# Kernel tuning notes

Measured on AMD Instinct MI355X. Metric: run time of the kernel, lower is better.

Reference implementation:

```python
import jax, jax.numpy as jnp
import numpy as np

ENC_DIM, DEC_DIM, ATT_DIM = 512, 512, 256
B, T = 64, 4096


def setup_inputs() -> dict:
    key = jax.random.key(0)
    ks = jax.random.split(key, 7)
    s_enc = 1.0 / np.sqrt(ENC_DIM)
    s_dec = 1.0 / np.sqrt(DEC_DIM)
    s_att = 1.0 / np.sqrt(ATT_DIM)
    return {
        "encoder_features": jax.random.normal(ks[0], (B, T, ENC_DIM), jnp.float32),
        "decoder_hidden": jax.random.normal(ks[1], (B, DEC_DIM), jnp.float32),
        # encoder_proj: Linear(encoder_dim, attention_dim) with bias
        "W_enc": jax.random.uniform(ks[2], (ENC_DIM, ATT_DIM), jnp.float32, -s_enc, s_enc),
        "b_enc": jax.random.uniform(ks[3], (ATT_DIM,), jnp.float32, -s_enc, s_enc),
        # decoder_proj: Linear(decoder_dim, attention_dim, bias=False)
        "W_dec": jax.random.uniform(ks[4], (DEC_DIM, ATT_DIM), jnp.float32, -s_dec, s_dec),
        # attention_vector: Linear(attention_dim, 1) with bias
        "v_att": jax.random.uniform(ks[5], (ATT_DIM,), jnp.float32, -s_att, s_att),
        "b_att": jax.random.uniform(ks[6], (), jnp.float32, -s_att, s_att),
    }


def reference(encoder_features, decoder_hidden, W_enc, b_enc, W_dec, v_att, b_att):
    # (B,T,A) = (B,T,E)@(E,A) + b
    enc_proj = jnp.einsum("bte,ea->bta", encoder_features, W_enc) + b_enc
    # (B,1,A)
    dec_proj = (decoder_hidden @ W_dec)[:, None, :]
    energy = jnp.tanh(enc_proj + dec_proj)                      # (B,T,A)
    scores = jnp.einsum("bta,a->bt", energy, v_att) + b_att     # (B,T)
    attention_weights = jax.nn.softmax(scores, axis=1)          # (B,T)
    context = jnp.einsum("bt,bte->be", attention_weights, encoder_features)
    return (context, attention_weights)
```

## Files before the change

kernel.cpp:

```cpp
#include <hip/hip_runtime.h>
#include <hip/hip_bf16.h>

#define E_DIM 512
#define D_DIM 512
#define A_DIM 256
#define B_SZ  64
#define T_SZ  4096
#define TT    64
#define NTB   (T_SZ / TT)
#define LDT   (E_DIM + 8)

typedef __bf16 bf16_t;
typedef bf16_t bf16x8 __attribute__((ext_vector_type(8)));
typedef float  f32x4  __attribute__((ext_vector_type(4)));

__device__ __forceinline__ unsigned short f2bf(float x) {
    union { float f; unsigned int u; } v; v.f = x;
    unsigned int u = v.u;
    return (unsigned short)((u + 0x7FFFu + ((u >> 16) & 1u)) >> 16);
}
__device__ __forceinline__ float bf_lo(unsigned int pk) {
    union { unsigned int u; float f; } v; v.u = pk << 16; return v.f;
}
__device__ __forceinline__ float bf_hi(unsigned int pk) {
    union { unsigned int u; float f; } v; v.u = pk & 0xFFFF0000u; return v.f;
}
__device__ __forceinline__ float tanh_fast(float x) {
    x = fminf(8.0f, fmaxf(-8.0f, x));
    float e = __expf(2.0f * x);
    return 1.0f - 2.0f * __builtin_amdgcn_rcpf(e + 1.0f);
}

__global__ __launch_bounds__(256) void prep_kernel(
    const float* __restrict__ dec, const float* __restrict__ W_enc,
    const float* __restrict__ b_enc, const float* __restrict__ W_dec,
    float* __restrict__ dp, unsigned short* __restrict__ Wt)
{
    const int bid = blockIdx.x, tid = threadIdx.x;
    if (bid < B_SZ) {
        float s = b_enc[tid];
        const float* dr = dec + bid * D_DIM;
        #pragma unroll 8
        for (int d = 0; d < D_DIM; ++d)
            s = fmaf(dr[d], W_dec[d * A_DIM + tid], s);
        dp[bid * A_DIM + tid] = s;
    } else {
        int base = (bid - B_SZ) * 2048;
        #pragma unroll
        for (int i = 0; i < 8; ++i) {
            int idx = base + tid + i * 256;
            int a = idx >> 9, e = idx & 511;
            Wt[idx] = f2bf(W_enc[e * A_DIM + a]);
        }
    }
}

__global__ __launch_bounds__(512, 4) void attn_main(
    const float* __restrict__ enc, const unsigned short* __restrict__ Wt,
    const float* __restrict__ dpg, const float* __restrict__ vatt,
    float* __restrict__ u_out, float* __restrict__ ctx_part)
{
    const int tb = blockIdx.x, b = blockIdx.y;
    const int tid = threadIdx.x;
    __shared__ unsigned short tile[TT * LDT];
    __shared__ float spart[8][TT];
    __shared__ float uu[TT];
    __shared__ float dp_s[A_DIM];
    __shared__ float vv[A_DIM];
    __shared__ float ctx_red[E_DIM];

    if (tid < A_DIM) {
        dp_s[tid] = dpg[b * A_DIM + tid];
        vv[tid]   = vatt[tid];
    }

    const float4* src = (const float4*)(enc + ((size_t)b * T_SZ + (size_t)tb * TT) * E_DIM);
    #pragma unroll 4
    for (int it = 0; it < 16; ++it) {
        int idx = tid + it * 512;
        int r = idx >> 7, c = idx & 127;
        float4 v4 = src[idx];
        ushort4 h;
        h.x = f2bf(v4.x); h.y = f2bf(v4.y); h.z = f2bf(v4.z); h.w = f2bf(v4.w);
        *(ushort4*)&tile[r * LDT + c * 4] = h;
    }
    __syncthreads();

    const int w = tid >> 6, lane = tid & 63;
    const int m16 = lane & 15, q = lane >> 4;
    f32x4 acc[4][2];
    #pragma unroll
    for (int mi = 0; mi < 4; ++mi)
        #pragma unroll
        for (int ni = 0; ni < 2; ++ni)
            acc[mi][ni] = (f32x4){0.f, 0.f, 0.f, 0.f};

    const unsigned short* WtW = Wt + (size_t)(w * 32) * E_DIM;
    #pragma unroll 2
    for (int k0 = 0; k0 < E_DIM; k0 += 32) {
        const int ka = k0 + q * 8;
        bf16x8 afr[4], bfr[2];
        #pragma unroll
        for (int ni = 0; ni < 2; ++ni)
            bfr[ni] = *(const bf16x8*)&WtW[(ni * 16 + m16) * E_DIM + ka];
        #pragma unroll
        for (int mi = 0; mi < 4; ++mi)
            afr[mi] = *(const bf16x8*)&tile[(mi * 16 + m16) * LDT + ka];
        #pragma unroll
        for (int mi = 0; mi < 4; ++mi)
            #pragma unroll
            for (int ni = 0; ni < 2; ++ni)
                acc[mi][ni] = __builtin_amdgcn_mfma_f32_16x16x32_bf16(
                    afr[mi], bfr[ni], acc[mi][ni], 0, 0, 0);
    }

    float va[2], dpv[2];
    #pragma unroll
    for (int ni = 0; ni < 2; ++ni) {
        int a = w * 32 + ni * 16 + m16;
        va[ni] = vv[a]; dpv[ni] = dp_s[a];
    }
    #pragma unroll
    for (int mi = 0; mi < 4; ++mi) {
        #pragma unroll
        for (int r = 0; r < 4; ++r) {
            float p = va[0] * tanh_fast(acc[mi][0][r] + dpv[0])
                    + va[1] * tanh_fast(acc[mi][1][r] + dpv[1]);
            p += __shfl_xor(p, 1); p += __shfl_xor(p, 2);
            p += __shfl_xor(p, 4); p += __shfl_xor(p, 8);
            if (m16 == 0) spart[w][mi * 16 + q * 4 + r] = p;
        }
    }
    __syncthreads();

    if (tid < TT) {
        float s = 0.f;
        #pragma unroll
        for (int w8 = 0; w8 < 8; ++w8) s += spart[w8][tid];
        float e = __expf(s);
        uu[tid] = e;
        u_out[(size_t)b * T_SZ + (size_t)tb * TT + tid] = e;
    }
    __syncthreads();

    {
        const int c2 = tid & 255, h = tid >> 8;
        float c0 = 0.f, c1 = 0.f;
        #pragma unroll 8
        for (int i = 0; i < 32; ++i) {
            int t = h * 32 + i;
            float ut = uu[t];
            unsigned int pk = *(const unsigned int*)&tile[t * LDT + 2 * c2];
            c0 = fmaf(ut, bf_lo(pk), c0);
            c1 = fmaf(ut, bf_hi(pk), c1);
        }
        if (h == 1) { ctx_red[2 * c2] = c0; ctx_red[2 * c2 + 1] = c1; }
        __syncthreads();
        if (h == 0) {
            c0 += ctx_red[2 * c2];
            c1 += ctx_red[2 * c2 + 1];
            float2 st; st.x = c0; st.y = c1;
            ((float2*)(ctx_part + ((size_t)tb * B_SZ + b) * E_DIM))[c2] = st;
        }
    }
}

__global__ __launch_bounds__(256) void finalize_kernel(
    const float* __restrict__ u, const float* __restrict__ ctx_part,
    float* __restrict__ out)
{
    const int b = blockIdx.x, tid = threadIdx.x;
    __shared__ float red[256];
    const float* ub = u + (size_t)b * T_SZ;
    float s = 0.f;
    for (int i = tid; i < T_SZ; i += 256) s += ub[i];
    red[tid] = s; __syncthreads();
    for (int st = 128; st > 0; st >>= 1) {
        if (tid < st) red[tid] += red[tid + st];
        __syncthreads();
    }
    const float invS = 1.0f / red[0];
    float* wout = out + B_SZ * E_DIM + (size_t)b * T_SZ;
    for (int i = tid; i < T_SZ; i += 256) wout[i] = ub[i] * invS;
    for (int e = tid; e < E_DIM; e += 256) {
        float c = 0.f;
        #pragma unroll 8
        for (int t = 0; t < NTB; ++t)
            c += ctx_part[((size_t)t * B_SZ + b) * E_DIM + e];
        out[(size_t)b * E_DIM + e] = c * invS;
    }
}

extern "C" void kernel_launch(void* const* d_in, const int* in_sizes, int n_in,
                              void* d_out, int out_size, void* d_ws, size_t ws_size,
                              hipStream_t stream) {
    const float* enc   = (const float*)d_in[0];
    const float* dec   = (const float*)d_in[1];
    const float* W_enc = (const float*)d_in[2];
    const float* b_enc = (const float*)d_in[3];
    const float* W_dec = (const float*)d_in[4];
    const float* v_att = (const float*)d_in[5];
    float* out = (float*)d_out;

    char* ws = (char*)d_ws;
    unsigned short* Wt = (unsigned short*)(ws);
    float* dp          = (float*)(ws + 262144);
    float* u           = (float*)(ws + 327680);
    float* ctx_part    = (float*)(ws + 1376256);

    prep_kernel<<<128, 256, 0, stream>>>(dec, W_enc, b_enc, W_dec, dp, Wt);
    attn_main<<<dim3(NTB, B_SZ), 512, 0, stream>>>(enc, Wt, dp, v_att, u, ctx_part);
    finalize_kernel<<<B_SZ, 256, 0, stream>>>(u, ctx_part, out);
}
```

Baseline: 836.3 us.

## Make attention blocks persistent over T slices with double-buffered tiles and atomic reduction

Each block now handles 16 consecutive 32-row tiles of one batch row instead of a single 64-row tile. The next tile's global load is issued into registers while the current tile is processed, then written into a double-buffered LDS tile. Context partials and the softmax denominator go to global memory through atomics, with zeroing done in prep, so the finalize kernel only scales. The grid drops to 512 blocks, which costs parallelism and latency hiding, and the float atomics make the summation order nondeterministic.

```diff
diff --git a/kernel.cpp b/kernel.cpp
--- a/kernel.cpp
+++ b/kernel.cpp
@@ -6,8 +6,10 @@
 #define A_DIM 256
 #define B_SZ  64
 #define T_SZ  4096
-#define TT    64
+#define TT    32
 #define NTB   (T_SZ / TT)
+#define TPB   16
+#define SLICES (NTB / TPB)
 #define LDT   (E_DIM + 8)
 
 typedef __bf16 bf16_t;
@@ -19,11 +21,8 @@
     unsigned int u = v.u;
     return (unsigned short)((u + 0x7FFFu + ((u >> 16) & 1u)) >> 16);
 }
-__device__ __forceinline__ float bf_lo(unsigned int pk) {
-    union { unsigned int u; float f; } v; v.u = pk << 16; return v.f;
-}
-__device__ __forceinline__ float bf_hi(unsigned int pk) {
-    union { unsigned int u; float f; } v; v.u = pk & 0xFFFF0000u; return v.f;
+__device__ __forceinline__ float bf2f(unsigned short h) {
+    union { unsigned int u; float f; } v; v.u = ((unsigned int)h) << 16; return v.f;
 }
 __device__ __forceinline__ float tanh_fast(float x) {
     x = fminf(8.0f, fmaxf(-8.0f, x));
@@ -34,7 +33,8 @@
 __global__ __launch_bounds__(256) void prep_kernel(
     const float* __restrict__ dec, const float* __restrict__ W_enc,
     const float* __restrict__ b_enc, const float* __restrict__ W_dec,
-    float* __restrict__ dp, unsigned short* __restrict__ Wt)
+    float* __restrict__ dp, unsigned short* __restrict__ Wt,
+    float* __restrict__ ctx_acc, float* __restrict__ S)
 {
     const int bid = blockIdx.x, tid = threadIdx.x;
     if (bid < B_SZ) {
@@ -44,6 +44,9 @@
         for (int d = 0; d < D_DIM; ++d)
             s = fmaf(dr[d], W_dec[d * A_DIM + tid], s);
         dp[bid * A_DIM + tid] = s;
+        ctx_acc[bid * E_DIM + tid]       = 0.0f;
+        ctx_acc[bid * E_DIM + 256 + tid] = 0.0f;
+        if (tid == 0) S[bid] = 0.0f;
     } else {
         int base = (bid - B_SZ) * 2048;
         #pragma unroll
@@ -58,136 +61,150 @@
 __global__ __launch_bounds__(512, 4) void attn_main(
     const float* __restrict__ enc, const unsigned short* __restrict__ Wt,
     const float* __restrict__ dpg, const float* __restrict__ vatt,
-    float* __restrict__ u_out, float* __restrict__ ctx_part)
+    float* __restrict__ u_out, float* __restrict__ ctx_acc,
+    float* __restrict__ S)
 {
-    const int tb = blockIdx.x, b = blockIdx.y;
+    const int p = blockIdx.x;
+    const int b = p >> 3, slice = p & 7;
     const int tid = threadIdx.x;
-    __shared__ unsigned short tile[TT * LDT];
+
+    __shared__ unsigned short tile[2][TT * LDT];
     __shared__ float spart[8][TT];
     __shared__ float uu[TT];
     __shared__ float dp_s[A_DIM];
     __shared__ float vv[A_DIM];
-    __shared__ float ctx_red[E_DIM];
 
     if (tid < A_DIM) {
         dp_s[tid] = dpg[b * A_DIM + tid];
         vv[tid]   = vatt[tid];
     }
 
-    const float4* src = (const float4*)(enc + ((size_t)b * T_SZ + (size_t)tb * TT) * E_DIM);
-    #pragma unroll 4
-    for (int it = 0; it < 16; ++it) {
-        int idx = tid + it * 512;
-        int r = idx >> 7, c = idx & 127;
-        float4 v4 = src[idx];
-        ushort4 h;
-        h.x = f2bf(v4.x); h.y = f2bf(v4.y); h.z = f2bf(v4.z); h.w = f2bf(v4.w);
-        *(ushort4*)&tile[r * LDT + c * 4] = h;
-    }
-    __syncthreads();
-
     const int w = tid >> 6, lane = tid & 63;
     const int m16 = lane & 15, q = lane >> 4;
-    f32x4 acc[4][2];
+
+    const float4* src0 = (const float4*)(enc +
+        ((size_t)b * T_SZ + (size_t)slice * TPB * TT) * E_DIM);
+
+    float4 r[8];
     #pragma unroll
-    for (int mi = 0; mi < 4; ++mi)
+    for (int it = 0; it < 8; ++it) r[it] = src0[tid + it * 512];
+    #pragma unroll
+    for (int it = 0; it < 8; ++it) {
+        int idx = tid + it * 512;
+        int rr = idx >> 7, cc = idx & 127;
+        ushort4 h;
+        h.x = f2bf(r[it].x); h.y = f2bf(r[it].y);
+        h.z = f2bf(r[it].z); h.w = f2bf(r[it].w);
+        *(ushort4*)&tile[0][rr * LDT + cc * 4] = h;
+    }
+    __syncthreads();
+
+    float va0, va1, dv0, dv1;
+    {
+        int a0 = w * 32 + m16;
+        va0 = vv[a0]; va1 = vv[a0 + 16];
+        dv0 = dp_s[a0]; dv1 = dp_s[a0 + 16];
+    }
+
+    const unsigned short* WtW = Wt + (size_t)(w * 32) * E_DIM;
+
+    float c_acc = 0.0f;
+    float sS    = 0.0f;
+
+    for (int i = 0; i < TPB; ++i) {
+        const int cur = i & 1, nxt = cur ^ 1;
+
+        if (i + 1 < TPB) {
+            const float4* srcn = src0 + (size_t)(i + 1) * 4096;
+            #pragma unroll
+            for (int it = 0; it < 8; ++it) r[it] = srcn[tid + it * 512];
+        }
+
+        f32x4 acc[2][2];
         #pragma unroll
-        for (int ni = 0; ni < 2; ++ni)
-            acc[mi][ni] = (f32x4){0.f, 0.f, 0.f, 0.f};
-
-    const unsigned short* WtW = Wt + (size_t)(w * 32) * E_DIM;
-    #pragma unroll 2
-    for (int k0 = 0; k0 < E_DIM; k0 += 32) {
-        const int ka = k0 + q * 8;
-        bf16x8 afr[4], bfr[2];
+        for (int mi = 0; mi < 2; ++mi)
+            #pragma unroll
+            for (int ni = 0; ni < 2; ++ni)
+                acc[mi][ni] = (f32x4){0.f, 0.f, 0.f, 0.f};
+
+        #pragma unroll 4
+        for (int k0 = 0; k0 < E_DIM; k0 += 32) {
+            const int ka = k0 + q * 8;
+            bf16x8 afr0 = *(const bf16x8*)&tile[cur][(m16) * LDT + ka];
+            bf16x8 afr1 = *(const bf16x8*)&tile[cur][(16 + m16) * LDT + ka];
+            bf16x8 bfr0 = *(const bf16x8*)&WtW[(m16) * E_DIM + ka];
+            bf16x8 bfr1 = *(const bf16x8*)&WtW[(16 + m16) * E_DIM + ka];
+            acc[0][0] = __builtin_amdgcn_mfma_f32_16x16x32_bf16(afr0, bfr0, acc[0][0], 0, 0, 0);
+            acc[0][1] = __builtin_amdgcn_mfma_f32_16x16x32_bf16(afr0, bfr1, acc[0][1], 0, 0, 0);
+            acc[1][0] = __builtin_amdgcn_mfma_f32_16x16x32_bf16(afr1, bfr0, acc[1][0], 0, 0, 0);
+            acc[1][1] = __builtin_amdgcn_mfma_f32_16x16x32_bf16(afr1, bfr1, acc[1][1], 0, 0, 0);
+        }
+
         #pragma unroll
-        for (int ni = 0; ni < 2; ++ni)
-            bfr[ni] = *(const bf16x8*)&WtW[(ni * 16 + m16) * E_DIM + ka];
-        #pragma unroll
-        for (int mi = 0; mi < 4; ++mi)
-            afr[mi] = *(const bf16x8*)&tile[(mi * 16 + m16) * LDT + ka];
-        #pragma unroll
-        for (int mi = 0; mi < 4; ++mi)
-            #pragma unroll
-            for (int ni = 0; ni < 2; ++ni)
-                acc[mi][ni] = __builtin_amdgcn_mfma_f32_16x16x32_bf16(
-                    afr[mi], bfr[ni], acc[mi][ni], 0, 0, 0);
-    }
-
-    float va[2], dpv[2];
+        for (int mi = 0; mi < 2; ++mi) {
+            #pragma unroll
+            for (int rr = 0; rr < 4; ++rr) {
+                float pv = va0 * tanh_fast(acc[mi][0][rr] + dv0)
+                         + va1 * tanh_fast(acc[mi][1][rr] + dv1);
+                pv += __shfl_xor(pv, 1); pv += __shfl_xor(pv, 2);
+                pv += __shfl_xor(pv, 4); pv += __shfl_xor(pv, 8);
+                if (m16 == 0) spart[w][mi * 16 + q * 4 + rr] = pv;
+            }
+        }
+        __syncthreads();
+
+        if (tid < TT) {
+            float s = 0.f;
+            #pragma unroll
+            for (int w8 = 0; w8 < 8; ++w8) s += spart[w8][tid];
+            float e = __expf(s);
+            uu[tid] = e;
+            sS += e;
+            u_out[(size_t)b * T_SZ + (size_t)(slice * TPB + i) * TT + tid] = e;
+        }
+        __syncthreads();
+
+        #pragma unroll 8
+        for (int t = 0; t < TT; ++t)
+            c_acc = fmaf(uu[t], bf2f(tile[cur][t * LDT + tid]), c_acc);
+
+        if (i + 1 < TPB) {
+            #pragma unroll
+            for (int it = 0; it < 8; ++it) {
+                int idx = tid + it * 512;
+                int rr = idx >> 7, cc = idx & 127;
+                ushort4 h;
+                h.x = f2bf(r[it].x); h.y = f2bf(r[it].y);
+                h.z = f2bf(r[it].z); h.w = f2bf(r[it].w);
+                *(ushort4*)&tile[nxt][rr * LDT + cc * 4] = h;
+            }
+        }
+        __syncthreads();
+    }
+
+    atomicAdd(&ctx_acc[(size_t)b * E_DIM + tid], c_acc);
+    if (w == 0) {
+        sS += __shfl_xor(sS, 1);  sS += __shfl_xor(sS, 2);
+        sS += __shfl_xor(sS, 4);  sS += __shfl_xor(sS, 8);
+        sS += __shfl_xor(sS, 16); sS += __shfl_xor(sS, 32);
+        if (lane == 0) atomicAdd(&S[b], sS);
+    }
+}
+
+__global__ __launch_bounds__(256) void finalize_kernel(
+    const float* __restrict__ u, const float* __restrict__ ctx_acc,
+    const float* __restrict__ S, float* __restrict__ out)
+{
+    const int b = blockIdx.x, j = blockIdx.y, tid = threadIdx.x;
+    const float invS = 1.0f / S[b];
+    const float* ub = u + (size_t)b * T_SZ + j * 1024;
+    float* wout = out + B_SZ * E_DIM + (size_t)b * T_SZ + j * 1024;
     #pragma unroll
-    for (int ni = 0; ni < 2; ++ni) {
-        int a = w * 32 + ni * 16 + m16;
-        va[ni] = vv[a]; dpv[ni] = dp_s[a];
-    }
-    #pragma unroll
-    for (int mi = 0; mi < 4; ++mi) {
-        #pragma unroll
-        for (int r = 0; r < 4; ++r) {
-            float p = va[0] * tanh_fast(acc[mi][0][r] + dpv[0])
-                    + va[1] * tanh_fast(acc[mi][1][r] + dpv[1]);
-            p += __shfl_xor(p, 1); p += __shfl_xor(p, 2);
-            p += __shfl_xor(p, 4); p += __shfl_xor(p, 8);
-            if (m16 == 0) spart[w][mi * 16 + q * 4 + r] = p;
-        }
-    }
-    __syncthreads();
-
-    if (tid < TT) {
-        float s = 0.f;
-        #pragma unroll
-        for (int w8 = 0; w8 < 8; ++w8) s += spart[w8][tid];
-        float e = __expf(s);
-        uu[tid] = e;
-        u_out[(size_t)b * T_SZ + (size_t)tb * TT + tid] = e;
-    }
-    __syncthreads();
-
-    {
-        const int c2 = tid & 255, h = tid >> 8;
-        float c0 = 0.f, c1 = 0.f;
-        #pragma unroll 8
-        for (int i = 0; i < 32; ++i) {
-            int t = h * 32 + i;
-            float ut = uu[t];
-            unsigned int pk = *(const unsigned int*)&tile[t * LDT + 2 * c2];
-            c0 = fmaf(ut, bf_lo(pk), c0);
-            c1 = fmaf(ut, bf_hi(pk), c1);
-        }
-        if (h == 1) { ctx_red[2 * c2] = c0; ctx_red[2 * c2 + 1] = c1; }
-        __syncthreads();
-        if (h == 0) {
-            c0 += ctx_red[2 * c2];
-            c1 += ctx_red[2 * c2 + 1];
-            float2 st; st.x = c0; st.y = c1;
-            ((float2*)(ctx_part + ((size_t)tb * B_SZ + b) * E_DIM))[c2] = st;
-        }
-    }
-}
-
-__global__ __launch_bounds__(256) void finalize_kernel(
-    const float* __restrict__ u, const float* __restrict__ ctx_part,
-    float* __restrict__ out)
-{
-    const int b = blockIdx.x, tid = threadIdx.x;
-    __shared__ float red[256];
-    const float* ub = u + (size_t)b * T_SZ;
-    float s = 0.f;
-    for (int i = tid; i < T_SZ; i += 256) s += ub[i];
-    red[tid] = s; __syncthreads();
-    for (int st = 128; st > 0; st >>= 1) {
-        if (tid < st) red[tid] += red[tid + st];
-        __syncthreads();
-    }
-    const float invS = 1.0f / red[0];
-    float* wout = out + B_SZ * E_DIM + (size_t)b * T_SZ;
-    for (int i = tid; i < T_SZ; i += 256) wout[i] = ub[i] * invS;
-    for (int e = tid; e < E_DIM; e += 256) {
-        float c = 0.f;
-        #pragma unroll 8
-        for (int t = 0; t < NTB; ++t)
-            c += ctx_part[((size_t)t * B_SZ + b) * E_DIM + e];
-        out[(size_t)b * E_DIM + e] = c * invS;
+    for (int it = 0; it < 4; ++it)
+        wout[tid + it * 256] = ub[tid + it * 256] * invS;
+    if (j == 0) {
+        out[(size_t)b * E_DIM + tid]       = ctx_acc[b * E_DIM + tid] * invS;
+        out[(size_t)b * E_DIM + 256 + tid] = ctx_acc[b * E_DIM + 256 + tid] * invS;
     }
 }
 
@@ -206,9 +223,10 @@
     unsigned short* Wt = (unsigned short*)(ws);
     float* dp          = (float*)(ws + 262144);
     float* u           = (float*)(ws + 327680);
-    float* ctx_part    = (float*)(ws + 1376256);
-
-    prep_kernel<<<128, 256, 0, stream>>>(dec, W_enc, b_enc, W_dec, dp, Wt);
-    attn_main<<<dim3(NTB, B_SZ), 512, 0, stream>>>(enc, Wt, dp, v_att, u, ctx_part);
-    finalize_kernel<<<B_SZ, 256, 0, stream>>>(u, ctx_part, out);
-}
+    float* ctx_acc     = (float*)(ws + 1376256);
+    float* S           = (float*)(ws + 1507328);
+
+    prep_kernel<<<128, 256, 0, stream>>>(dec, W_enc, b_enc, W_dec, dp, Wt, ctx_acc, S);
+    attn_main<<<B_SZ * SLICES, 512, 0, stream>>>(enc, Wt, dp, v_att, u, ctx_acc, S);
+    finalize_kernel<<<dim3(B_SZ, 4), 256, 0, stream>>>(u, ctx_acc, S, out);
+}
```

Result: slower. 893.6 us (+6.8%).
